# Optimization experiments

Hardware: AMD Instinct MI355X
Metric: run time of the kernel (lower is better)

The kernel has to match this reference:

```python
import jax, jax.numpy as jnp
import numpy as np
from jax import lax

B, L, H = 256, 256, 128
K_MIN, K_MAX, ITERS = 2, 8, 3
ALPHA, BETA = 0.5, 0.5
EPS8, EPS9 = 1e-8, 1e-9


def setup_inputs() -> dict:
    key = jax.random.key(0)
    k1, k2, k3 = jax.random.split(key, 3)
    user_features = jax.random.normal(k1, (B, L, H), dtype=jnp.float32)
    W = jax.random.normal(k2, (H, H), dtype=jnp.float32) * (1.0 / np.sqrt(H))
    b_init = jax.random.normal(k3, (B, K_MAX, L), dtype=jnp.float32)
    return {"user_features": user_features, "W": W, "b_init": b_init}


def _cap_scale(cap):
    # squash-style scalar: n/(1+n)/sqrt(n+eps), n = ||cap||^2
    n = jnp.sum(cap * cap, axis=-1, keepdims=True)
    return n / (1.0 + n) / jnp.sqrt(n + EPS9)


def reference(user_features, W, b_init):
    e = user_features                                  # [B,L,H]
    hat = e @ W.T                                      # nn.Linear(H,H,bias=False)
    # repeat over capsules then transpose -> every capsule sees same projection
    hat_k = jnp.broadcast_to(hat[:, None, :, :], (B, K_MAX, L, H))
    hat_iter = lax.stop_gradient(hat_k)                # stop_grad=True path

    b = b_init
    cap = None
    c = None
    for t in range(ITERS):
        c = jax.nn.softmax(b, axis=-1)                 # mask is all ones
        if t < ITERS - 1:
            cap = jnp.einsum('bkl,bklh->bkh', c, hat_iter)
            cap = _cap_scale(cap) * cap
            delta = jnp.einsum('bklh,bkh->bkl', hat_iter, cap)
            b = b + delta
        else:
            cap = jnp.einsum('bkl,bklh->bkh', c, hat_k)
            cap = _cap_scale(cap) * cap
    interest_capsule = cap                             # [B,K,H]
    final_c = c                                        # [B,K,L]

    e_norm = e / (jnp.linalg.norm(e, axis=-1, keepdims=True) + EPS8)
    strength = jnp.linalg.norm(interest_capsule, axis=-1)  # [B,K]

    scores = []
    for k in range(K_MIN, K_MAX + 1):
        _, idx = lax.top_k(strength, k)                # [B,k]
        c_k = jnp.take_along_axis(final_c, idx[:, :, None], axis=1)  # [B,k,L]
        denom = c_k.sum(axis=-1, keepdims=True) + EPS8
        mu_k = jnp.einsum('bkl,blh->bkh', c_k, e) / denom
        mu_n = mu_k / (jnp.linalg.norm(mu_k, axis=-1, keepdims=True) + EPS8)
        cos = jnp.einsum('blh,bkh->bkl', e_norm, mu_n)
        consistency = (c_k * cos).sum(axis=(-1, -2)) / float(max(1, k) * max(1, L))
        if k > 1:
            pair = jnp.einsum('bkh,bjh->bkj', mu_n, mu_n)
            upper = jnp.triu(pair, k=1).sum(axis=(-1, -2))
            diversity = 1.0 - (2.0 / (k * (k - 1))) * upper
        else:
            diversity = jnp.ones((B,), dtype=mu_n.dtype)
        scores.append(ALPHA * consistency + BETA * diversity)

    k_scores = jnp.stack(scores, axis=1)               # [B, K_MAX-K_MIN+1]
    optimal_k = jnp.argmax(k_scores, axis=1) + K_MIN   # [B]
    return optimal_k, k_scores
```

## Files before the change

kernel.cpp:

```cpp
#include <hip/hip_runtime.h>
#include <hip/hip_bf16.h>
#include <math.h>

#define NB 256
#define NL 256
#define NH 128
#define NK 8

typedef __attribute__((ext_vector_type(8))) short bf16x8;
typedef __attribute__((ext_vector_type(4))) short s16x4;
typedef __attribute__((ext_vector_type(4))) float f32x4;

static __device__ __forceinline__ short f2bf(float x) {
    __hip_bfloat16 b = __float2bfloat16(x);
    return *reinterpret_cast<short*>(&b);
}
static __device__ __forceinline__ float bf2f(short s) {
    union { unsigned int u; float f; } v;
    v.u = ((unsigned int)(unsigned short)s) << 16;
    return v.f;
}

#define MFMA __builtin_amdgcn_mfma_f32_16x16x32_bf16

__global__ __launch_bounds__(256) void setup_w_kernel(const float* __restrict__ W,
                                                      short* __restrict__ whi,
                                                      short* __restrict__ wlo,
                                                      short* __restrict__ wthi,
                                                      short* __restrict__ wtlo) {
    const int id = blockIdx.x * 256 + threadIdx.x;
    const int h = id >> 7, j = id & 127;
    const float w = W[id];
    const short hi = f2bf(w);
    const short lo = f2bf(w - bf2f(hi));
    whi[id] = hi;
    wlo[id] = lo;
    wthi[j * 128 + h] = hi;
    wtlo[j * 128 + h] = lo;
}

__global__ __launch_bounds__(1024) void fused_kernel(const float* __restrict__ e,
                                                     const float* __restrict__ b_init,
                                                     const short* __restrict__ whi,
                                                     const short* __restrict__ wlo,
                                                     const short* __restrict__ wthi,
                                                     const short* __restrict__ wtlo,
                                                     float* __restrict__ out) {
    const int b = blockIdx.x;
    const int t = threadIdx.x;
    const int lane = t & 63, wv = t >> 6;
    const int l16 = lane & 15, grp = lane >> 4;

    __shared__ __align__(16) short eThi[128 * 264];
    __shared__ __align__(16) short eTlo[128 * 264];
    __shared__ __align__(16) short cax[16 * 264];
    __shared__ __align__(16) short mpk[16 * 136];
    __shared__ __align__(16) short cappk[16 * 136];
    __shared__ __align__(16) short gpk[16 * 136];
    __shared__ float enl[256];
    __shared__ float red32[128];
    __shared__ float svals[8], strv[8], Ps[28];

    float* capb = (float*)gpk;

    const float* ebg = e + (size_t)b * (NL * NH);

    bf16x8 eah[4], eal[4];
    {
        const int row = wv * 16 + l16;
        float ss = 0.f;
#pragma unroll
        for (int ks = 0; ks < 4; ++ks) {
            const float4 f0 = *(const float4*)&ebg[row * 128 + ks * 32 + grp * 8];
            const float4 f1 = *(const float4*)&ebg[row * 128 + ks * 32 + grp * 8 + 4];
            const float fx[8] = {f0.x, f0.y, f0.z, f0.w, f1.x, f1.y, f1.z, f1.w};
            bf16x8 hv, lv;
#pragma unroll
            for (int j = 0; j < 8; ++j) {
                const short h = f2bf(fx[j]);
                hv[j] = h;
                lv[j] = f2bf(fx[j] - bf2f(h));
                ss += fx[j] * fx[j];
            }
            eah[ks] = hv;
            eal[ks] = lv;
        }
        ss += __shfl_xor(ss, 16);
        ss += __shfl_xor(ss, 32);
        if (grp == 0) enl[wv * 16 + l16] = sqrtf(ss) + 1e-8f;
    }

#pragma unroll
    for (int i = 0; i < 4; ++i) {
        const int p = i * 1024 + t;
        const int h = p & 127, c = p >> 7;
        float le[8];
#pragma unroll
        for (int j = 0; j < 8; ++j) le[j] = ebg[(c * 8 + j) * 128 + h];
        bf16x8 hv, lv;
#pragma unroll
        for (int j = 0; j < 8; ++j) {
            const short s = f2bf(le[j]);
            hv[j] = s;
            lv[j] = f2bf(le[j] - bf2f(s));
        }
        *(bf16x8*)&eThi[h * 264 + c * 8] = hv;
        *(bf16x8*)&eTlo[h * 264 + c * 8] = lv;
    }

    float lr0 = 0.f, lr1 = 0.f, lr2 = 0.f, lr3 = 0.f;
    if (l16 < 8) {
        const float4 bi = *(const float4*)&b_init[(size_t)b * 2048 + l16 * 256 + wv * 16 + grp * 4];
        lr0 = bi.x; lr1 = bi.y; lr2 = bi.z; lr3 = bi.w;
    }
    __syncthreads();

    for (int iter = 0; iter < 3; ++iter) {
        {
            const float e0 = expf(lr0), e1 = expf(lr1);
            const float e2 = expf(lr2), e3 = expf(lr3);
            float s4 = e0 + e1 + e2 + e3;
            s4 += __shfl_xor(s4, 16);
            s4 += __shfl_xor(s4, 32);
            if (l16 < 8 && grp == 0) red32[wv * 8 + l16] = s4;
            __syncthreads();
            float ksum = 0.f;
#pragma unroll
            for (int w = 0; w < 16; ++w) ksum += red32[w * 8 + (l16 & 7)];
            const float inv = 1.0f / ksum;
            if (l16 < 8) {
                const int lb = wv * 16 + grp * 4;
                const float cv[4] = {e0 * inv, e1 * inv, e2 * inv, e3 * inv};
                s16x4 his, los;
#pragma unroll
                for (int j = 0; j < 4; ++j) {
                    const short h = f2bf(cv[j]);
                    his[j] = h;
                    los[j] = f2bf(cv[j] - bf2f(h));
                }
                *(s16x4*)&cax[l16 * 264 + lb] = his;
                *(s16x4*)&cax[(l16 + 8) * 264 + lb] = los;
            }
            __syncthreads();
        }

        if (wv < 8) {
            const int n0 = wv * 16;
            f32x4 acc = (f32x4){0.f, 0.f, 0.f, 0.f};
#pragma unroll
            for (int ks = 0; ks < 8; ++ks) {
                const bf16x8 af = *(const bf16x8*)&cax[l16 * 264 + ks * 32 + grp * 8];
                const bf16x8 bh = *(const bf16x8*)&eThi[(n0 + l16) * 264 + ks * 32 + grp * 8];
                const bf16x8 bl = *(const bf16x8*)&eTlo[(n0 + l16) * 264 + ks * 32 + grp * 8];
                acc = MFMA(af, bh, acc, 0, 0, 0);
                acc = MFMA(af, bl, acc, 0, 0, 0);
            }
            f32x4 ms;
#pragma unroll
            for (int r = 0; r < 4; ++r) ms[r] = acc[r] + __shfl_xor(acc[r], 32);
            if (grp < 2) {
#pragma unroll
                for (int r = 0; r < 4; ++r) {
                    const int k = grp * 4 + r, h = n0 + l16;
                    const short hv = f2bf(ms[r]);
                    mpk[k * 136 + h] = hv;
                    mpk[(k + 8) * 136 + h] = f2bf(ms[r] - bf2f(hv));
                }
            }
        }
        __syncthreads();

        if (wv < 8) {
            const int n0 = wv * 16;
            f32x4 acc = (f32x4){0.f, 0.f, 0.f, 0.f};
#pragma unroll
            for (int ks = 0; ks < 4; ++ks) {
                const bf16x8 af = *(const bf16x8*)&mpk[l16 * 136 + ks * 32 + grp * 8];
                const int bo = (n0 + l16) * 128 + ks * 32 + grp * 8;
                acc = MFMA(af, *(const bf16x8*)&whi[bo], acc, 0, 0, 0);
                acc = MFMA(af, *(const bf16x8*)&wlo[bo], acc, 0, 0, 0);
            }
            f32x4 cs;
#pragma unroll
            for (int r = 0; r < 4; ++r) cs[r] = acc[r] + __shfl_xor(acc[r], 32);
            if (grp < 2) {
#pragma unroll
                for (int r = 0; r < 4; ++r)
                    capb[(grp * 4 + r) * 136 + n0 + l16] = cs[r];
            }
        }
        __syncthreads();

        if (wv < 8) {
            const int k = wv;
            float x0 = capb[k * 136 + lane], x1 = capb[k * 136 + 64 + lane];
            float s = x0 * x0 + x1 * x1;
#pragma unroll
            for (int o = 32; o; o >>= 1) s += __shfl_xor(s, o);
            const float sc = s / (1.0f + s) / sqrtf(s + 1e-9f);
            x0 *= sc; x1 *= sc;
            short hv = f2bf(x0);
            cappk[k * 136 + lane] = hv;
            cappk[(k + 8) * 136 + lane] = f2bf(x0 - bf2f(hv));
            hv = f2bf(x1);
            cappk[k * 136 + 64 + lane] = hv;
            cappk[(k + 8) * 136 + 64 + lane] = f2bf(x1 - bf2f(hv));
            if (iter == 2 && lane == 0)
                strv[k] = s / (1.0f + s) * sqrtf(s) / sqrtf(s + 1e-9f);
        }
        __syncthreads();

        if (iter < 2) {
            if (wv < 8) {
                const int n0 = wv * 16;
                f32x4 acc = (f32x4){0.f, 0.f, 0.f, 0.f};
#pragma unroll
                for (int ks = 0; ks < 4; ++ks) {
                    const bf16x8 af = *(const bf16x8*)&cappk[l16 * 136 + ks * 32 + grp * 8];
                    const int bo = (n0 + l16) * 128 + ks * 32 + grp * 8;
                    acc = MFMA(af, *(const bf16x8*)&wthi[bo], acc, 0, 0, 0);
                    acc = MFMA(af, *(const bf16x8*)&wtlo[bo], acc, 0, 0, 0);
                }
                f32x4 gs;
#pragma unroll
                for (int r = 0; r < 4; ++r) gs[r] = acc[r] + __shfl_xor(acc[r], 32);
                if (grp < 2) {
#pragma unroll
                    for (int r = 0; r < 4; ++r) {
                        const int k = grp * 4 + r, h = n0 + l16;
                        const short hv = f2bf(gs[r]);
                        gpk[k * 136 + h] = hv;
                        gpk[(k + 8) * 136 + h] = f2bf(gs[r] - bf2f(hv));
                    }
                }
            }
            __syncthreads();

            {
                f32x4 acc;
                acc[0] = (l16 < 8) ? lr0 : 0.f;
                acc[1] = (l16 < 8) ? lr1 : 0.f;
                acc[2] = (l16 < 8) ? lr2 : 0.f;
                acc[3] = (l16 < 8) ? lr3 : 0.f;
#pragma unroll
                for (int ks = 0; ks < 4; ++ks) {
                    const bf16x8 bf = *(const bf16x8*)&gpk[l16 * 136 + ks * 32 + grp * 8];
                    acc = MFMA(eah[ks], bf, acc, 0, 0, 0);
                    acc = MFMA(eal[ks], bf, acc, 0, 0, 0);
                }
                lr0 = acc[0] + __shfl_xor(acc[0], 8);
                lr1 = acc[1] + __shfl_xor(acc[1], 8);
                lr2 = acc[2] + __shfl_xor(acc[2], 8);
                lr3 = acc[3] + __shfl_xor(acc[3], 8);
            }
        }
    }

    if (wv < 8) {
        const int k = wv;
        float x0 = bf2f(mpk[k * 136 + lane]) + bf2f(mpk[(k + 8) * 136 + lane]);
        float x1 = bf2f(mpk[k * 136 + 64 + lane]) + bf2f(mpk[(k + 8) * 136 + 64 + lane]);
        float s = x0 * x0 + x1 * x1;
#pragma unroll
        for (int o = 32; o; o >>= 1) s += __shfl_xor(s, o);
        const float nv = sqrtf(s) + 1e-8f;
        x0 /= nv; x1 /= nv;
        short hv = f2bf(x0);
        gpk[k * 136 + lane] = hv;
        gpk[(k + 8) * 136 + lane] = f2bf(x0 - bf2f(hv));
        hv = f2bf(x1);
        gpk[k * 136 + 64 + lane] = hv;
        gpk[(k + 8) * 136 + 64 + lane] = f2bf(x1 - bf2f(hv));
    }
    __syncthreads();

    {
        f32x4 acc = (f32x4){0.f, 0.f, 0.f, 0.f};
#pragma unroll
        for (int ks = 0; ks < 4; ++ks) {
            const bf16x8 bf = *(const bf16x8*)&gpk[l16 * 136 + ks * 32 + grp * 8];
            acc = MFMA(eah[ks], bf, acc, 0, 0, 0);
            acc = MFMA(eal[ks], bf, acc, 0, 0, 0);
        }
        f32x4 d;
#pragma unroll
        for (int r = 0; r < 4; ++r) d[r] = acc[r] + __shfl_xor(acc[r], 8);
        float sv = 0.f;
        if (l16 < 8) {
#pragma unroll
            for (int r = 0; r < 4; ++r) {
                const int l = wv * 16 + grp * 4 + r;
                const float cv = bf2f(cax[l16 * 264 + l]) + bf2f(cax[(l16 + 8) * 264 + l]);
                sv += d[r] * cv / enl[l];
            }
        }
        sv += __shfl_xor(sv, 16);
        sv += __shfl_xor(sv, 32);
        if (l16 < 8 && grp == 0) red32[wv * 8 + l16] = sv;
    }

#pragma unroll
    for (int pp = 0; pp < 2; ++pp) {
        const int p = wv + pp * 16;
        if (p < 28) {
            int i = 0, rem = p;
            while (rem >= 7 - i) { rem -= 7 - i; ++i; }
            const int j = i + 1 + rem;
            const float mi0 = bf2f(gpk[i * 136 + lane]) + bf2f(gpk[(i + 8) * 136 + lane]);
            const float mi1 = bf2f(gpk[i * 136 + 64 + lane]) + bf2f(gpk[(i + 8) * 136 + 64 + lane]);
            const float mj0 = bf2f(gpk[j * 136 + lane]) + bf2f(gpk[(j + 8) * 136 + lane]);
            const float mj1 = bf2f(gpk[j * 136 + 64 + lane]) + bf2f(gpk[(j + 8) * 136 + 64 + lane]);
            float v = mi0 * mj0 + mi1 * mj1;
#pragma unroll
            for (int o = 32; o; o >>= 1) v += __shfl_xor(v, o);
            if (lane == 0) Ps[p] = v;
        }
    }
    __syncthreads();
    if (t < 8) {
        float s = 0.f;
#pragma unroll
        for (int w = 0; w < 16; ++w) s += red32[w * 8 + t];
        svals[t] = s;
    }
    __syncthreads();

    if (t == 0) {
        int idx[8];
        for (int i = 0; i < 8; ++i) idx[i] = i;
        for (int a = 1; a < 8; ++a) {
            const int key = idx[a];
            const float kv = strv[key];
            int bb = a - 1;
            while (bb >= 0 && strv[idx[bb]] < kv) { idx[bb + 1] = idx[bb]; --bb; }
            idx[bb + 1] = key;
        }
        float best = -1e30f;
        int bestk = 2;
        float cons_sum = 0.f, pair_sum = 0.f;
        for (int kk = 1; kk <= 8; ++kk) {
            const int ni = idx[kk - 1];
            cons_sum += svals[ni];
            for (int a = 0; a < kk - 1; ++a) {
                const int ia = idx[a];
                const int lo = ia < ni ? ia : ni;
                const int hi2 = ia < ni ? ni : ia;
                const int off0 = lo * 7 - lo * (lo - 1) / 2;
                pair_sum += Ps[off0 + hi2 - lo - 1];
            }
            if (kk >= 2) {
                const float cons = cons_sum / (kk * 256.0f);
                const float divv = 1.0f - (2.0f / (kk * (kk - 1))) * pair_sum;
                const float score = 0.5f * cons + 0.5f * divv;
                out[256 + b * 7 + (kk - 2)] = score;
                if (score > best) { best = score; bestk = kk; }
            }
        }
        out[b] = (float)bestk;
    }
}

extern "C" void kernel_launch(void* const* d_in, const int* in_sizes, int n_in,
                              void* d_out, int out_size, void* d_ws, size_t ws_size,
                              hipStream_t stream) {
    const float* e = (const float*)d_in[0];
    const float* W = (const float*)d_in[1];
    const float* b_init = (const float*)d_in[2];
    float* out = (float*)d_out;

    short* whi = (short*)d_ws;
    short* wlo = whi + 16384;
    short* wthi = wlo + 16384;
    short* wtlo = wthi + 16384;

    hipLaunchKernelGGL(setup_w_kernel, dim3(64), dim3(256), 0, stream, W, whi, wlo, wthi, wtlo);
    hipLaunchKernelGGL(fused_kernel, dim3(NB), dim3(1024), 0, stream,
                       e, b_init, whi, wlo, wthi, wtlo, out);
}
```

Before: 39.54 us.

## Defer softmax and squash normalization to cut barriers; preload W fragments into registers

Softmax is no longer normalized before the c·e^T MFMA. The per-capsule 1/sum is applied after the product, and the squash norm is computed from partial sums in the same pass, which removes two __syncthreads per routing iteration and the separate capsule-scale stage. W and W^T bf16 hi/lo fragments are loaded into registers once per block instead of being reloaded from global memory every iteration. Unnormalized exponentials stored as bf16 hi/lo may change rounding slightly. The extra register arrays raise VGPR pressure.

```diff
diff --git a/kernel.cpp b/kernel.cpp
--- a/kernel.cpp
+++ b/kernel.cpp
@@ -59,11 +59,22 @@
     __shared__ __align__(16) short gpk[16 * 136];
     __shared__ float enl[256];
     __shared__ float red32[128];
-    __shared__ float svals[8], strv[8], Ps[28];
-
-    float* capb = (float*)gpk;
+    __shared__ __align__(16) float nrmp[64];
+    __shared__ float ksf[8], svals[8], strv[8], Ps[28];
 
     const float* ebg = e + (size_t)b * (NL * NH);
+
+    bf16x8 wh3[4], wl3[4], wh5[4], wl5[4];
+    if (wv < 8) {
+#pragma unroll
+        for (int ks = 0; ks < 4; ++ks) {
+            const int bo = (wv * 16 + l16) * 128 + ks * 32 + grp * 8;
+            wh3[ks] = *(const bf16x8*)&whi[bo];
+            wl3[ks] = *(const bf16x8*)&wlo[bo];
+            wh5[ks] = *(const bf16x8*)&wthi[bo];
+            wl5[ks] = *(const bf16x8*)&wtlo[bo];
+        }
+    }
 
     bf16x8 eah[4], eal[4];
     {
@@ -87,7 +98,7 @@
         }
         ss += __shfl_xor(ss, 16);
         ss += __shfl_xor(ss, 32);
-        if (grp == 0) enl[wv * 16 + l16] = sqrtf(ss) + 1e-8f;
+        if (grp == 0) enl[row] = sqrtf(ss) + 1e-8f;
     }
 
 #pragma unroll
@@ -123,14 +134,9 @@
             s4 += __shfl_xor(s4, 16);
             s4 += __shfl_xor(s4, 32);
             if (l16 < 8 && grp == 0) red32[wv * 8 + l16] = s4;
-            __syncthreads();
-            float ksum = 0.f;
-#pragma unroll
-            for (int w = 0; w < 16; ++w) ksum += red32[w * 8 + (l16 & 7)];
-            const float inv = 1.0f / ksum;
             if (l16 < 8) {
                 const int lb = wv * 16 + grp * 4;
-                const float cv[4] = {e0 * inv, e1 * inv, e2 * inv, e3 * inv};
+                const float cv[4] = {e0, e1, e2, e3};
                 s16x4 his, los;
 #pragma unroll
                 for (int j = 0; j < 4; ++j) {
@@ -141,8 +147,8 @@
                 *(s16x4*)&cax[l16 * 264 + lb] = his;
                 *(s16x4*)&cax[(l16 + 8) * 264 + lb] = los;
             }
-            __syncthreads();
-        }
+        }
+        __syncthreads();
 
         if (wv < 8) {
             const int n0 = wv * 16;
@@ -171,59 +177,75 @@
         __syncthreads();
 
         if (wv < 8) {
+            float inv = 0.f;
+            if (l16 < 8) {
+                float kss = 0.f;
+#pragma unroll
+                for (int w = 0; w < 16; ++w) kss += red32[w * 8 + l16];
+                inv = 1.0f / kss;
+            }
             const int n0 = wv * 16;
             f32x4 acc = (f32x4){0.f, 0.f, 0.f, 0.f};
 #pragma unroll
             for (int ks = 0; ks < 4; ++ks) {
                 const bf16x8 af = *(const bf16x8*)&mpk[l16 * 136 + ks * 32 + grp * 8];
-                const int bo = (n0 + l16) * 128 + ks * 32 + grp * 8;
-                acc = MFMA(af, *(const bf16x8*)&whi[bo], acc, 0, 0, 0);
-                acc = MFMA(af, *(const bf16x8*)&wlo[bo], acc, 0, 0, 0);
+                acc = MFMA(af, wh3[ks], acc, 0, 0, 0);
+                acc = MFMA(af, wl3[ks], acc, 0, 0, 0);
             }
             f32x4 cs;
-#pragma unroll
-            for (int r = 0; r < 4; ++r) cs[r] = acc[r] + __shfl_xor(acc[r], 32);
-            if (grp < 2) {
-#pragma unroll
-                for (int r = 0; r < 4; ++r)
-                    capb[(grp * 4 + r) * 136 + n0 + l16] = cs[r];
-            }
-        }
-        __syncthreads();
-
-        if (wv < 8) {
-            const int k = wv;
-            float x0 = capb[k * 136 + lane], x1 = capb[k * 136 + 64 + lane];
-            float s = x0 * x0 + x1 * x1;
-#pragma unroll
-            for (int o = 32; o; o >>= 1) s += __shfl_xor(s, o);
-            const float sc = s / (1.0f + s) / sqrtf(s + 1e-9f);
-            x0 *= sc; x1 *= sc;
-            short hv = f2bf(x0);
-            cappk[k * 136 + lane] = hv;
-            cappk[(k + 8) * 136 + lane] = f2bf(x0 - bf2f(hv));
-            hv = f2bf(x1);
-            cappk[k * 136 + 64 + lane] = hv;
-            cappk[(k + 8) * 136 + 64 + lane] = f2bf(x1 - bf2f(hv));
-            if (iter == 2 && lane == 0)
-                strv[k] = s / (1.0f + s) * sqrtf(s) / sqrtf(s + 1e-9f);
+            float pn[4];
+#pragma unroll
+            for (int r = 0; r < 4; ++r) {
+                cs[r] = acc[r] + __shfl_xor(acc[r], 32);
+                cs[r] *= __shfl(inv, grp * 4 + r);
+                float p2 = cs[r] * cs[r];
+                p2 += __shfl_xor(p2, 1);
+                p2 += __shfl_xor(p2, 2);
+                p2 += __shfl_xor(p2, 4);
+                p2 += __shfl_xor(p2, 8);
+                pn[r] = p2;
+            }
+            if (l16 == 0 && grp < 2) {
+                float4 pv;
+                pv.x = pn[0]; pv.y = pn[1]; pv.z = pn[2]; pv.w = pn[3];
+                *(float4*)&nrmp[wv * 8 + grp * 4] = pv;
+            }
+            if (iter < 2 && grp < 2) {
+#pragma unroll
+                for (int r = 0; r < 4; ++r) {
+                    const int k = grp * 4 + r, h = n0 + l16;
+                    const short hv = f2bf(cs[r]);
+                    cappk[k * 136 + h] = hv;
+                    cappk[(k + 8) * 136 + h] = f2bf(cs[r] - bf2f(hv));
+                }
+            }
+            if (iter == 2 && wv == 0 && grp == 0 && l16 < 8) ksf[l16] = inv;
         }
         __syncthreads();
 
         if (iter < 2) {
             if (wv < 8) {
+                float sc = 0.f;
+                if (l16 < 8) {
+                    float n = 0.f;
+#pragma unroll
+                    for (int w = 0; w < 8; ++w) n += nrmp[w * 8 + l16];
+                    sc = n / (1.0f + n) / sqrtf(n + 1e-9f);
+                }
                 const int n0 = wv * 16;
                 f32x4 acc = (f32x4){0.f, 0.f, 0.f, 0.f};
 #pragma unroll
                 for (int ks = 0; ks < 4; ++ks) {
                     const bf16x8 af = *(const bf16x8*)&cappk[l16 * 136 + ks * 32 + grp * 8];
-                    const int bo = (n0 + l16) * 128 + ks * 32 + grp * 8;
-                    acc = MFMA(af, *(const bf16x8*)&wthi[bo], acc, 0, 0, 0);
-                    acc = MFMA(af, *(const bf16x8*)&wtlo[bo], acc, 0, 0, 0);
+                    acc = MFMA(af, wh5[ks], acc, 0, 0, 0);
+                    acc = MFMA(af, wl5[ks], acc, 0, 0, 0);
                 }
                 f32x4 gs;
 #pragma unroll
-                for (int r = 0; r < 4; ++r) gs[r] = acc[r] + __shfl_xor(acc[r], 32);
+                for (int r = 0; r < 4; ++r) {
+                    gs[r] = acc[r] + __shfl_xor(acc[r], 32);
+                    gs[r] *= __shfl(sc, grp * 4 + r);
+                }
                 if (grp < 2) {
 #pragma unroll
                     for (int r = 0; r < 4; ++r) {
@@ -256,6 +278,12 @@
         }
     }
 
+    if (wv == 8 && lane < 8) {
+        float n = 0.f;
+#pragma unroll
+        for (int w = 0; w < 8; ++w) n += nrmp[w * 8 + lane];
+        strv[lane] = n / (1.0f + n) * sqrtf(n) / sqrtf(n + 1e-9f);
+    }
     if (wv < 8) {
         const int k = wv;
         float x0 = bf2f(mpk[k * 136 + lane]) + bf2f(mpk[(k + 8) * 136 + lane]);
@@ -287,10 +315,11 @@
         for (int r = 0; r < 4; ++r) d[r] = acc[r] + __shfl_xor(acc[r], 8);
         float sv = 0.f;
         if (l16 < 8) {
+            const float kinv = ksf[l16];
 #pragma unroll
             for (int r = 0; r < 4; ++r) {
                 const int l = wv * 16 + grp * 4 + r;
-                const float cv = bf2f(cax[l16 * 264 + l]) + bf2f(cax[(l16 + 8) * 264 + l]);
+                const float cv = (bf2f(cax[l16 * 264 + l]) + bf2f(cax[(l16 + 8) * 264 + l])) * kinv;
                 sv += d[r] * cv / enl[l];
             }
         }
@@ -298,7 +327,6 @@
         sv += __shfl_xor(sv, 32);
         if (l16 < 8 && grp == 0) red32[wv * 8 + l16] = sv;
     }
-
 #pragma unroll
     for (int pp = 0; pp < 2; ++pp) {
         const int p = wv + pp * 16;
```

Result: slower. 46.32 us (+17.2%).
